# Kernel optimization log

Hardware: AMD Instinct MI355X
Metric: run time of the kernel (lower is better)

## Reference

```python
import jax, jax.numpy as jnp
import numpy as np

WAVE_LEN = 1000.0
DIM_G = 64


def box_relational_embedding(boxes):
    # boxes: (B, N, 4) -> (B, N, N, 64) trigonometric geometry embedding
    B, N, _ = boxes.shape
    x_min, y_min, x_max, y_max = jnp.split(boxes, 4, axis=-1)  # each (B,N,1)
    cx = (x_min + x_max) * 0.5
    cy = (y_min + y_max) * 0.5
    w = (x_max - x_min) + 1.0
    h = (y_max - y_min) + 1.0
    cxT = jnp.swapaxes(cx, 1, 2)  # (B,1,N)
    cyT = jnp.swapaxes(cy, 1, 2)
    dx = jnp.log(jnp.clip(jnp.abs((cx - cxT) / w), 1e-3))  # (B,N,N)
    dy = jnp.log(jnp.clip(jnp.abs((cy - cyT) / h), 1e-3))
    dw = jnp.log(w / jnp.swapaxes(w, 1, 2))
    dh = jnp.log(h / jnp.swapaxes(h, 1, 2))
    pos = jnp.stack([dx, dy, dw, dh], axis=-1)  # (B,N,N,4)
    n_freq = DIM_G // 8  # 8 frequency bands
    dim_mat = 1.0 / (WAVE_LEN ** (jnp.arange(n_freq, dtype=pos.dtype) / n_freq))
    mul = (100.0 * pos)[..., None] * dim_mat  # (B,N,N,4,8)
    mul = mul.reshape(B, N, N, 4 * n_freq)  # (B,N,N,32)
    return jnp.concatenate([jnp.sin(mul), jnp.cos(mul)], axis=-1)  # (B,N,N,64)


def setup_inputs() -> dict:
    key = jax.random.key(0)
    ks = jax.random.split(key, 12)
    B, N, D, H = 32, 196, 1024, 8
    scale = 0.02
    inp = {
        "input_query": jax.random.normal(ks[0], (B, N, D), jnp.float32),
        "input_key": jax.random.normal(ks[1], (B, N, D), jnp.float32),
        "input_value": jax.random.normal(ks[2], (B, N, D), jnp.float32),
        "input_box": jax.random.uniform(ks[3], (B, N, 4), jnp.float32),
        "Wq": jax.random.normal(ks[4], (D, D), jnp.float32) * scale,
        "bq": jnp.zeros((D,), jnp.float32),
        "Wk": jax.random.normal(ks[5], (D, D), jnp.float32) * scale,
        "bk": jnp.zeros((D,), jnp.float32),
        "Wv": jax.random.normal(ks[6], (D, D), jnp.float32) * scale,
        "bv": jnp.zeros((D,), jnp.float32),
        "Wo": jax.random.normal(ks[7], (D, D), jnp.float32) * scale,
        "bo": jnp.zeros((D,), jnp.float32),
        "WG_w": jax.random.normal(ks[8], (H, DIM_G), jnp.float32) * scale,  # 8 stacked (64->1) linears
        "WG_b": jnp.zeros((H,), jnp.float32),
    }
    return inp


def reference(input_query, input_key, input_value, input_box,
              Wq, bq, Wk, bk, Wv, bv, Wo, bo, WG_w, WG_b):
    B, N, D = input_query.shape
    H = WG_w.shape[0]
    dk = D // H
    # relation geometry weights per head: (B,H,N,N)
    geo = box_relational_embedding(input_box)  # (B,N,N,64)
    wg = jax.nn.relu(jnp.einsum('bnmg,hg->bhnm', geo, WG_w) + WG_b[None, :, None, None])
    # projections (torch Linear: x @ W.T + b), reshape to (B,H,N,dk)
    def proj(x, W, b):
        return (x @ W.T + b).reshape(B, N, H, dk).transpose(0, 2, 1, 3)
    q = proj(input_query, Wq, bq)
    k = proj(input_key, Wk, bk)
    v = proj(input_value, Wv, bv)
    scores = jnp.einsum('bhnd,bhmd->bhnm', q, k) / np.sqrt(dk).astype(q.dtype)
    logits = jnp.log(jnp.clip(wg, 1e-6)) + scores
    attn = jax.nn.softmax(logits, axis=-1)  # (B,H,N,N)
    out = jnp.einsum('bhnm,bhmd->bhnd', attn, v)  # (B,H,N,dk)
    out = out.transpose(0, 2, 1, 3).reshape(B, N, D)
    return out @ Wo.T + bo
```

## Files before the change

kernel.cpp:

```cpp
#include <hip/hip_runtime.h>
#include <hip/hip_bf16.h>

typedef __bf16 bf16;
typedef _Float16 half_t;
typedef bf16 bf16x8 __attribute__((ext_vector_type(8)));
typedef bf16 bf16x4 __attribute__((ext_vector_type(4)));
typedef float floatx4 __attribute__((ext_vector_type(4)));

#define B_ 32
#define N_ 196
#define H_ 8
#define D_ 1024
#define DK_ 128
#define BN_ (B_ * N_)
#define BH_ (B_ * H_)
#define NPAD_ 224
#define PSTRIDE_ 232

#define KT3_ 32

typedef __attribute__((address_space(3))) unsigned int lds_uint;
typedef const __attribute__((address_space(1))) unsigned int glb_uint;

__device__ __forceinline__ void async_copy16(const bf16* g, bf16* l) {
  __builtin_amdgcn_global_load_lds((glb_uint*)g, (lds_uint*)l, 16, 0, 0);
}

#define BARRIER() asm volatile("s_barrier" ::: "memory")
#define WAITV0() asm volatile("s_waitcnt vmcnt(0)" ::: "memory")
#define WAITV4() asm volatile("s_waitcnt vmcnt(4)" ::: "memory")

__global__ __launch_bounds__(256) void cvt3_kernel(const float* __restrict__ s0,
                                                   const float* __restrict__ s1,
                                                   const float* __restrict__ s2,
                                                   bf16* __restrict__ d0,
                                                   bf16* __restrict__ d1,
                                                   bf16* __restrict__ d2, int n4) {
  const int which = blockIdx.y;
  const float* s = (which == 0) ? s0 : (which == 1) ? s1 : s2;
  bf16* d = (which == 0) ? d0 : (which == 1) ? d1 : d2;
  int i = blockIdx.x * 256 + threadIdx.x;
  if (i >= n4) return;
  float4 v = ((const float4*)s)[i];
  bf16x4 o;
  o[0] = (bf16)v.x;
  o[1] = (bf16)v.y;
  o[2] = (bf16)v.z;
  o[3] = (bf16)v.w;
  *(bf16x4*)(d + (size_t)i * 4) = o;
}

__global__ __launch_bounds__(256) void cvt4_kernel(const float* __restrict__ s0,
                                                   const float* __restrict__ s1,
                                                   const float* __restrict__ s2,
                                                   const float* __restrict__ s3,
                                                   bf16* __restrict__ d0,
                                                   bf16* __restrict__ d1,
                                                   bf16* __restrict__ d2,
                                                   bf16* __restrict__ d3, int n4) {
  const int which = blockIdx.y;
  const float* s = (which == 0) ? s0 : (which == 1) ? s1 : (which == 2) ? s2 : s3;
  bf16* d = (which == 0) ? d0 : (which == 1) ? d1 : (which == 2) ? d2 : d3;
  int i = blockIdx.x * 256 + threadIdx.x;
  if (i >= n4) return;
  float4 v = ((const float4*)s)[i];
  bf16x4 o;
  o[0] = (bf16)v.x;
  o[1] = (bf16)v.y;
  o[2] = (bf16)v.z;
  o[3] = (bf16)v.w;
  *(bf16x4*)(d + (size_t)i * 4) = o;
}

__global__ __launch_bounds__(256) void geo_kernel(const float* __restrict__ box,
                                                  const float* __restrict__ WGw,
                                                  const float* __restrict__ WGb,
                                                  half_t* __restrict__ S) {
  __shared__ float4 wsh[128];
  if (threadIdx.x < 128) wsh[threadIdx.x] = ((const float4*)WGw)[threadIdx.x];
  __syncthreads();

  int tid = blockIdx.x * 256 + threadIdx.x;
  int b = tid / (N_ * N_);
  int rem = tid - b * (N_ * N_);
  int n = rem / N_;
  int m = rem - n * N_;

  float4 bn = ((const float4*)box)[b * N_ + n];
  float4 bm = ((const float4*)box)[b * N_ + m];
  float cxn = (bn.x + bn.z) * 0.5f, cyn = (bn.y + bn.w) * 0.5f;
  float wn = bn.z - bn.x + 1.0f, hn = bn.w - bn.y + 1.0f;
  float cxm = (bm.x + bm.z) * 0.5f, cym = (bm.y + bm.w) * 0.5f;
  float wm = bm.z - bm.x + 1.0f, hm = bm.w - bm.y + 1.0f;

  float pos[4];
  pos[0] = __logf(fmaxf(fabsf((cxn - cxm) / wn), 1e-3f));
  pos[1] = __logf(fmaxf(fabsf((cyn - cym) / hn), 1e-3f));
  pos[2] = __logf(wn / wm);
  pos[3] = __logf(hn / hm);

  const float dims[8] = {1.0f,          0.4216965034f, 0.1778279410f, 0.0749894209f,
                         0.0316227766f, 0.0133352143f, 0.0056234133f, 0.0023713737f};
  float feat[64];
#pragma unroll
  for (int p = 0; p < 4; p++) {
#pragma unroll
    for (int f = 0; f < 8; f++) {
      float a = 100.0f * pos[p] * dims[f];
      feat[p * 8 + f] = __sinf(a);
      feat[32 + p * 8 + f] = __cosf(a);
    }
  }
#pragma unroll
  for (int hh = 0; hh < 8; hh++) {
    float accv = WGb[hh];
#pragma unroll
    for (int g4 = 0; g4 < 16; g4++) {
      float4 wv = wsh[hh * 16 + g4];
      accv += feat[g4 * 4 + 0] * wv.x + feat[g4 * 4 + 1] * wv.y +
              feat[g4 * 4 + 2] * wv.z + feat[g4 * 4 + 3] * wv.w;
    }
    S[((size_t)((b * H_ + hh) * N_ + n)) * NPAD_ + m] = (half_t)fmaxf(accv, 1e-6f);
  }
}

template <int VARIANT>
__global__ __launch_bounds__(256, 3) void gemm3b(
    const bf16* __restrict__ A0, const bf16* __restrict__ A1, const bf16* __restrict__ A2,
    const bf16* __restrict__ W0, const bf16* __restrict__ W1, const bf16* __restrict__ W2,
    const float* __restrict__ b0, const float* __restrict__ b1, const float* __restrict__ b2,
    void* __restrict__ O0, void* __restrict__ O1, void* __restrict__ O2) {
  __shared__ bf16 As[3][128 * 32];
  __shared__ bf16 Bs[3][128 * 32];

  const int z = (VARIANT == 0) ? blockIdx.z : 0;
  const bf16* A = (z == 0) ? A0 : (z == 1) ? A1 : A2;
  const bf16* W = (z == 0) ? W0 : (z == 1) ? W1 : W2;
  const float* bias = (z == 0) ? b0 : (z == 1) ? b1 : b2;

  const int tid = threadIdx.x;
  const int lane = tid & 63;
  const int wid = tid >> 6;
  const int l16 = lane & 15;
  const int quad = lane >> 4;
  const int wm = wid >> 1;
  const int wn = wid & 1;

  const bf16* gA = A + (size_t)blockIdx.y * 128 * D_;
  const bf16* gB = W + (size_t)blockIdx.x * 128 * D_;

  size_t sOff[2];
  int sDst[2];
#pragma unroll
  for (int u = 0; u < 2; u++) {
    const int slot = u * 256 + tid;
    const int srow = slot >> 2;
    const int scs = slot & 3;
    sOff[u] = (size_t)srow * D_ + (size_t)((scs ^ (srow & 3)) * 8);
    sDst[u] = slot * 8;
  }

  int arow[4], brow[4];
#pragma unroll
  for (int i = 0; i < 4; i++) arow[i] = (wm * 64 + i * 16 + l16) * 32;
#pragma unroll
  for (int j = 0; j < 4; j++) brow[j] = (wn * 64 + j * 16 + l16) * 32;
  const int kslot = (quad ^ (l16 & 3)) * 8;

  floatx4 acc[4][4];
#pragma unroll
  for (int i = 0; i < 4; i++)
#pragma unroll
    for (int j = 0; j < 4; j++)
#pragma unroll
      for (int r = 0; r < 4; r++) acc[i][j][r] = 0.0f;

#pragma unroll
  for (int kt = 0; kt < 2; kt++) {
    const bf16* sa = gA + kt * 32;
    const bf16* sb = gB + kt * 32;
#pragma unroll
    for (int u = 0; u < 2; u++) {
      async_copy16(sa + sOff[u], &As[kt][sDst[u]]);
      async_copy16(sb + sOff[u], &Bs[kt][sDst[u]]);
    }
  }
  WAITV4();
  BARRIER();

  for (int kt = 0; kt < KT3_; ++kt) {
    const int g = kt % 3;
    const bool pf = (kt + 2 < KT3_);
    if (pf) {
      const int gn = (kt + 2) % 3;
      const bf16* pa = gA + (kt + 2) * 32;
      const bf16* pb = gB + (kt + 2) * 32;
#pragma unroll
      for (int u = 0; u < 2; u++) {
        async_copy16(pa + sOff[u], &As[gn][sDst[u]]);
        async_copy16(pb + sOff[u], &Bs[gn][sDst[u]]);
      }
    }
    const bf16* Ab = As[g];
    const bf16* Bb = Bs[g];
    bf16x8 af[4], bfv[4];
#pragma unroll
    for (int i = 0; i < 4; i++) af[i] = *(const bf16x8*)(Ab + arow[i] + kslot);
#pragma unroll
    for (int j = 0; j < 4; j++) bfv[j] = *(const bf16x8*)(Bb + brow[j] + kslot);
    __builtin_amdgcn_s_setprio(1);
#pragma unroll
    for (int i = 0; i < 4; i++)
#pragma unroll
      for (int j = 0; j < 4; j++)
        acc[i][j] = __builtin_amdgcn_mfma_f32_16x16x32_bf16(af[i], bfv[j], acc[i][j], 0, 0, 0);
    __builtin_amdgcn_s_setprio(0);
    if (kt < KT3_ - 1) {
      if (pf) WAITV4();
      else    WAITV0();
      BARRIER();
    }
  }

  const int m0 = blockIdx.y * 128 + wm * 64;
  const int n0 = blockIdx.x * 128 + wn * 64;
#pragma unroll
  for (int j = 0; j < 4; j++) {
    const int col = n0 + j * 16 + l16;
    const float bv = bias[col];
#pragma unroll
    for (int i = 0; i < 4; i++) {
#pragma unroll
      for (int r = 0; r < 4; r++) {
        const int row = m0 + i * 16 + quad * 4 + r;
        float v = acc[i][j][r] + bv;
        if (VARIANT == 1) {
          ((float*)O0)[(size_t)row * D_ + col] = v;
        } else if (z < 2) {
          bf16* Cout = z ? (bf16*)O1 : (bf16*)O0;
          Cout[(size_t)row * D_ + col] = (bf16)v;
        } else {
          int b = row / N_;
          int n = row - b * N_;
          int h = col >> 7;
          int d = col & (DK_ - 1);
          ((bf16*)O2)[((size_t)((b * H_ + h) * DK_ + d)) * NPAD_ + n] = (bf16)v;
        }
      }
    }
  }
}

__global__ __launch_bounds__(256) void attn_kernel(const bf16* __restrict__ Q,
                                                   const bf16* __restrict__ Kmat,
                                                   const bf16* __restrict__ Vt,
                                                   const half_t* __restrict__ Sb,
                                                   bf16* __restrict__ AO) {
  __shared__ alignas(16) char smem[46080];
  bf16* KsB[2] = {(bf16*)smem, (bf16*)smem + 4096};
  bf16* Pl = (bf16*)smem;
  bf16* VsB[2] = {(bf16*)(smem + 29696), (bf16*)(smem + 29696) + 4096};

  const int f = blockIdx.x;
  const int tile = (f >> 3) & 3;
  const int bh = (f & 7) | ((f >> 5) << 3);
  const int b = bh >> 3;
  const int h = bh & 7;
  const int tid = threadIdx.x;
  const int wave = tid >> 6;
  const int lane = tid & 63;
  const int l16 = lane & 15;
  const int quad = lane >> 4;
  const int nrb = tile * 64 + wave * 16;

  size_t kSrc[2];
  int kDst[2];
#pragma unroll
  for (int u = 0; u < 2; u++) {
    const int slot = u * 256 + tid;
    const int srow = slot >> 4;
    const int scs = slot & 15;
    kSrc[u] = (size_t)(b * N_ + srow) * D_ + h * DK_ + (scs ^ (srow & 7)) * 8;
    kDst[u] = slot * 8;
  }
  size_t vSrc[2];
#pragma unroll
  for (int u = 0; u < 2; u++) {
    const int slot = u * 256 + tid;
    const int vrow = slot >> 2;
    const int vcs = slot & 3;
    vSrc[u] = (size_t)bh * DK_ * NPAD_ + (size_t)vrow * NPAD_ + (vcs ^ (vrow & 3)) * 8;
  }

#pragma unroll
  for (int u = 0; u < 2; u++) async_copy16(Kmat + kSrc[u], KsB[0] + kDst[u]);

  const int na = nrb + l16;
  const bool nav = na < N_;
  const bf16* aptr = Q + ((size_t)(b * N_ + (nav ? na : 0))) * D_ + h * DK_ + quad * 8;
  bf16x8 afr[4];
#pragma unroll
  for (int kk = 0; kk < 4; kk++) {
    bf16x8 v = *(const bf16x8*)(aptr + kk * 32);
    if (!nav) {
#pragma unroll
      for (int e = 0; e < 8; e++) v[e] = (bf16)0.0f;
    }
    afr[kk] = v;
  }
  WAITV0();
  BARRIER();

  floatx4 S[14];
#pragma unroll
  for (int j = 0; j < 14; j++)
#pragma unroll
    for (int r = 0; r < 4; r++) S[j][r] = 0.0f;

  for (int jt = 0; jt < 7; ++jt) {
    const int cur = jt & 1;
    if (jt < 6) {
      const size_t koff = (size_t)((jt + 1) * 32) * D_;
#pragma unroll
      for (int u = 0; u < 2; u++)
        async_copy16(Kmat + kSrc[u] + koff, KsB[cur ^ 1] + kDst[u]);
    }
    const bf16* Kb = KsB[cur];
    __builtin_amdgcn_s_setprio(1);
#pragma unroll
    for (int jj = 0; jj < 2; jj++) {
      const int mloc = jj * 16 + l16;
#pragma unroll
      for (int kk = 0; kk < 4; kk++) {
        bf16x8 bb = *(const bf16x8*)(Kb + mloc * 128 + ((kk * 4 + quad) ^ (l16 & 7)) * 8);
        S[jt * 2 + jj] = __builtin_amdgcn_mfma_f32_16x16x32_bf16(afr[kk], bb, S[jt * 2 + jj], 0, 0, 0);
      }
    }
    __builtin_amdgcn_s_setprio(0);
    if (jt < 6) {
      WAITV0();
      BARRIER();
    }
  }

#pragma unroll
  for (int u = 0; u < 2; u++) async_copy16(Vt + vSrc[u], VsB[0] + kDst[u]);

  BARRIER();

  const float scale = 0.08838834764831845f;
  const half_t* bbase = Sb + ((size_t)bh * N_) * NPAD_;
  bf16* pw = Pl + wave * 16 * PSTRIDE_;
  float inv[4];
#pragma unroll
  for (int r = 0; r < 4; r++) {
    const int n = nrb + quad * 4 + r;
    const bool nv = n < N_;
    const size_t brow = (size_t)(nv ? n : 0) * NPAD_;
    float mx = -1e30f;
#pragma unroll
    for (int j = 0; j < 14; j++) {
      const int m = j * 16 + l16;
      float s = (nv && m < N_) ? S[j][r] * scale : -1e30f;
      S[j][r] = s;
      mx = fmaxf(mx, s);
    }
#pragma unroll
    for (int off = 1; off < 16; off <<= 1) mx = fmaxf(mx, __shfl_xor(mx, off, 64));
    float sum = 0.0f;
#pragma unroll
    for (int j = 0; j < 14; j++) {
      const int m = j * 16 + l16;
      float w = (m < N_) ? (float)bbase[brow + m] : 0.0f;
      float e = w * __expf(S[j][r] - mx);
      sum += e;
      pw[(quad * 4 + r) * PSTRIDE_ + m] = (bf16)e;
    }
#pragma unroll
    for (int off = 1; off < 16; off <<= 1) sum += __shfl_xor(sum, off, 64);
    inv[r] = 1.0f / sum;
  }
  __syncthreads();

  floatx4 O[8];
#pragma unroll
  for (int j2 = 0; j2 < 8; j2++)
#pragma unroll
    for (int r = 0; r < 4; r++) O[j2][r] = 0.0f;

  const bf16* pr = pw + l16 * PSTRIDE_ + quad * 8;
  for (int t7 = 0; t7 < 7; ++t7) {
    const int cur = t7 & 1;
    if (t7 < 6) {
      const size_t voff = (size_t)((t7 + 1) * 32);
#pragma unroll
      for (int u = 0; u < 2; u++)
        async_copy16(Vt + vSrc[u] + voff, VsB[cur ^ 1] + kDst[u]);
    }
    const bf16* Vb = VsB[cur];
    bf16x8 a = *(const bf16x8*)(pr + t7 * 32);
    __builtin_amdgcn_s_setprio(1);
#pragma unroll
    for (int j2 = 0; j2 < 8; j2++) {
      bf16x8 bb = *(const bf16x8*)(Vb + (j2 * 16 + l16) * 32 + (quad ^ (l16 & 3)) * 8);
      O[j2] = __builtin_amdgcn_mfma_f32_16x16x32_bf16(a, bb, O[j2], 0, 0, 0);
    }
    __builtin_amdgcn_s_setprio(0);
    if (t7 < 6) {
      WAITV0();
      BARRIER();
    }
  }

#pragma unroll
  for (int r = 0; r < 4; r++) {
    const int n = nrb + quad * 4 + r;
    if (n < N_) {
#pragma unroll
      for (int j2 = 0; j2 < 8; j2++) {
        AO[((size_t)(b * N_ + n)) * D_ + h * DK_ + j2 * 16 + l16] = (bf16)(O[j2][r] * inv[r]);
      }
    }
  }
}

extern "C" void kernel_launch(void* const* d_in, const int* in_sizes, int n_in,
                              void* d_out, int out_size, void* d_ws, size_t ws_size,
                              hipStream_t stream) {
  const float* xq = (const float*)d_in[0];
  const float* xk = (const float*)d_in[1];
  const float* xv = (const float*)d_in[2];
  const float* box = (const float*)d_in[3];
  const float* Wq = (const float*)d_in[4];
  const float* bq = (const float*)d_in[5];
  const float* Wk = (const float*)d_in[6];
  const float* bk = (const float*)d_in[7];
  const float* Wv = (const float*)d_in[8];
  const float* bv = (const float*)d_in[9];
  const float* Wo = (const float*)d_in[10];
  const float* bo = (const float*)d_in[11];
  const float* WGw = (const float*)d_in[12];
  const float* WGb = (const float*)d_in[13];

  size_t off = 0;
  char* wsc = (char*)d_ws;
  auto alloc = [&](size_t bytes) -> void* {
    void* p = wsc + off;
    off += (bytes + 255) & ~(size_t)255;
    return p;
  };
  bf16* xq_b = (bf16*)alloc((size_t)BN_ * D_ * 2);
  bf16* xk_b = (bf16*)alloc((size_t)BN_ * D_ * 2);
  bf16* xv_b = (bf16*)alloc((size_t)BN_ * D_ * 2);
  bf16* wq_b = (bf16*)alloc((size_t)D_ * D_ * 2);
  bf16* wk_b = (bf16*)alloc((size_t)D_ * D_ * 2);
  bf16* wv_b = (bf16*)alloc((size_t)D_ * D_ * 2);
  bf16* wo_b = (bf16*)alloc((size_t)D_ * D_ * 2);
  bf16* q_b = (bf16*)alloc((size_t)BN_ * D_ * 2);
  bf16* k_b = (bf16*)alloc((size_t)BN_ * D_ * 2);
  bf16* vt_b = (bf16*)alloc((size_t)BH_ * DK_ * NPAD_ * 2);
  bf16* ao_b = (bf16*)alloc((size_t)BN_ * D_ * 2);
  half_t* S = (half_t*)alloc((size_t)BH_ * N_ * NPAD_ * 2);

  const int n4x = BN_ * D_ / 4;
  const int n4w = D_ * D_ / 4;
  dim3 g3(n4x / 256, 3, 1);
  cvt3_kernel<<<g3, 256, 0, stream>>>(xq, xk, xv, xq_b, xk_b, xv_b, n4x);
  dim3 g4(n4w / 256, 4, 1);
  cvt4_kernel<<<g4, 256, 0, stream>>>(Wq, Wk, Wv, Wo, wq_b, wk_b, wv_b, wo_b, n4w);

  geo_kernel<<<(B_ * N_ * N_) / 256, 256, 0, stream>>>(box, WGw, WGb, S);

  hipMemsetAsync(vt_b, 0, (size_t)BH_ * DK_ * NPAD_ * 2, stream);

  dim3 gqkv(D_ / 128, BN_ / 128, 3);
  gemm3b<0><<<gqkv, 256, 0, stream>>>(xq_b, xk_b, xv_b, wq_b, wk_b, wv_b, bq, bk, bv,
                                      q_b, k_b, vt_b);

  attn_kernel<<<1024, 256, 0, stream>>>(q_b, k_b, vt_b, S, ao_b);

  dim3 gout(D_ / 128, BN_ / 128, 1);
  gemm3b<1><<<gout, 256, 0, stream>>>(ao_b, nullptr, nullptr, wo_b, nullptr, nullptr,
                                      bo, nullptr, nullptr, d_out, nullptr, nullptr);
}
```

Measured before the change: 320.0 us.

## Rework GEMM pipeline to double-buffered K=64 tiles with XCD-aware block remap

The projection GEMMs drop the triple-buffered K=32 pipeline in favour of double-buffered K=64 tiles. That halves the number of barrier and wait rounds, and the next tile's global-to-LDS copies are split across the two MFMA halves of each iteration. Blocks are also remapped so that consecutive hardware block IDs, which are dealt round-robin across XCDs, land on contiguous tile ranges, aiming at better L2 reuse. The cost is more LDS per block and lower occupancy (launch bounds drop from 3 to 2 blocks per CU), plus a full vmcnt(0) wait each iteration.

Measured after the change: 315.0 us. Within noise of the previous version (-1.6%).

```diff
diff --git a/kernel.cpp b/kernel.cpp
--- a/kernel.cpp
+++ b/kernel.cpp
@@ -17,7 +17,7 @@
 #define NPAD_ 224
 #define PSTRIDE_ 232
 
-#define KT3_ 32
+#define KT_ 16
 
 typedef __attribute__((address_space(3))) unsigned int lds_uint;
 typedef const __attribute__((address_space(1))) unsigned int glb_uint;
@@ -28,7 +28,6 @@
 
 #define BARRIER() asm volatile("s_barrier" ::: "memory")
 #define WAITV0() asm volatile("s_waitcnt vmcnt(0)" ::: "memory")
-#define WAITV4() asm volatile("s_waitcnt vmcnt(4)" ::: "memory")
 
 __global__ __launch_bounds__(256) void cvt3_kernel(const float* __restrict__ s0,
                                                    const float* __restrict__ s1,
@@ -125,15 +124,23 @@
 }
 
 template <int VARIANT>
-__global__ __launch_bounds__(256, 3) void gemm3b(
+__global__ __launch_bounds__(256, 2) void gemm2p(
     const bf16* __restrict__ A0, const bf16* __restrict__ A1, const bf16* __restrict__ A2,
     const bf16* __restrict__ W0, const bf16* __restrict__ W1, const bf16* __restrict__ W2,
     const float* __restrict__ b0, const float* __restrict__ b1, const float* __restrict__ b2,
     void* __restrict__ O0, void* __restrict__ O1, void* __restrict__ O2) {
-  __shared__ bf16 As[3][128 * 32];
-  __shared__ bf16 Bs[3][128 * 32];
-
-  const int z = (VARIANT == 0) ? blockIdx.z : 0;
+  __shared__ bf16 As[2][128 * 64];
+  __shared__ bf16 Bs[2][128 * 64];
+
+  const int NZ = (VARIANT == 0) ? 3 : 1;
+  const int chunk = 49 * NZ;
+  const int f = blockIdx.x + (blockIdx.y << 3) + blockIdx.z * 392;
+  const int L = (f & 7) * chunk + (f >> 3);
+  const int lx = L & 7;
+  const int lyz = L >> 3;
+  const int ly = (VARIANT == 0) ? (lyz % 49) : lyz;
+  const int z = (VARIANT == 0) ? (lyz / 49) : 0;
+
   const bf16* A = (z == 0) ? A0 : (z == 1) ? A1 : A2;
   const bf16* W = (z == 0) ? W0 : (z == 1) ? W1 : W2;
   const float* bias = (z == 0) ? b0 : (z == 1) ? b1 : b2;
@@ -146,26 +153,22 @@
   const int wm = wid >> 1;
   const int wn = wid & 1;
 
-  const bf16* gA = A + (size_t)blockIdx.y * 128 * D_;
-  const bf16* gB = W + (size_t)blockIdx.x * 128 * D_;
-
-  size_t sOff[2];
-  int sDst[2];
-#pragma unroll
-  for (int u = 0; u < 2; u++) {
-    const int slot = u * 256 + tid;
-    const int srow = slot >> 2;
-    const int scs = slot & 3;
-    sOff[u] = (size_t)srow * D_ + (size_t)((scs ^ (srow & 3)) * 8);
-    sDst[u] = slot * 8;
-  }
-
-  int arow[4], brow[4];
-#pragma unroll
-  for (int i = 0; i < 4; i++) arow[i] = (wm * 64 + i * 16 + l16) * 32;
-#pragma unroll
-  for (int j = 0; j < 4; j++) brow[j] = (wn * 64 + j * 16 + l16) * 32;
-  const int kslot = (quad ^ (l16 & 3)) * 8;
+  const bf16* gA = A + (size_t)ly * 128 * D_;
+  const bf16* gB = W + (size_t)lx * 128 * D_;
+
+  const int srow = tid >> 3;
+  const int lslot = (tid & 7) ^ (srow & 7);
+  size_t sOff[4];
+#pragma unroll
+  for (int u = 0; u < 4; u++) sOff[u] = (size_t)(u * 32 + srow) * D_ + lslot * 8;
+
+  int arow[4], brow[4], kslot[2];
+#pragma unroll
+  for (int i = 0; i < 4; i++) arow[i] = (wm * 64 + i * 16 + l16) * 64;
+#pragma unroll
+  for (int j = 0; j < 4; j++) brow[j] = (wn * 64 + j * 16 + l16) * 64;
+#pragma unroll
+  for (int kk = 0; kk < 2; kk++) kslot[kk] = ((kk * 4 + quad) ^ (l16 & 7)) * 8;
 
   floatx4 acc[4][4];
 #pragma unroll
@@ -176,38 +179,32 @@
       for (int r = 0; r < 4; r++) acc[i][j][r] = 0.0f;
 
 #pragma unroll
-  for (int kt = 0; kt < 2; kt++) {
-    const bf16* sa = gA + kt * 32;
-    const bf16* sb = gB + kt * 32;
-#pragma unroll
-    for (int u = 0; u < 2; u++) {
-      async_copy16(sa + sOff[u], &As[kt][sDst[u]]);
-      async_copy16(sb + sOff[u], &Bs[kt][sDst[u]]);
-    }
-  }
-  WAITV4();
+  for (int u = 0; u < 4; u++) {
+    async_copy16(gA + sOff[u], &As[0][u * 2048 + tid * 8]);
+    async_copy16(gB + sOff[u], &Bs[0][u * 2048 + tid * 8]);
+  }
+  WAITV0();
   BARRIER();
 
-  for (int kt = 0; kt < KT3_; ++kt) {
-    const int g = kt % 3;
-    const bool pf = (kt + 2 < KT3_);
+  for (int kt = 0; kt < KT_; ++kt) {
+    const int cur = kt & 1;
+    const bf16* Ab = As[cur];
+    const bf16* Bb = Bs[cur];
+    const bool pf = (kt + 1 < KT_);
+    const bf16* pa = gA + (kt + 1) * 64;
+    const bf16* pb = gB + (kt + 1) * 64;
+    bf16* dA = As[cur ^ 1];
+    bf16* dB = Bs[cur ^ 1];
+    bf16x8 af[4], bfv[4];
+
+#pragma unroll
+    for (int i = 0; i < 4; i++) af[i] = *(const bf16x8*)(Ab + arow[i] + kslot[0]);
+#pragma unroll
+    for (int j = 0; j < 4; j++) bfv[j] = *(const bf16x8*)(Bb + brow[j] + kslot[0]);
     if (pf) {
-      const int gn = (kt + 2) % 3;
-      const bf16* pa = gA + (kt + 2) * 32;
-      const bf16* pb = gB + (kt + 2) * 32;
-#pragma unroll
-      for (int u = 0; u < 2; u++) {
-        async_copy16(pa + sOff[u], &As[gn][sDst[u]]);
-        async_copy16(pb + sOff[u], &Bs[gn][sDst[u]]);
-      }
-    }
-    const bf16* Ab = As[g];
-    const bf16* Bb = Bs[g];
-    bf16x8 af[4], bfv[4];
-#pragma unroll
-    for (int i = 0; i < 4; i++) af[i] = *(const bf16x8*)(Ab + arow[i] + kslot);
-#pragma unroll
-    for (int j = 0; j < 4; j++) bfv[j] = *(const bf16x8*)(Bb + brow[j] + kslot);
+#pragma unroll
+      for (int u = 0; u < 4; u++) async_copy16(pa + sOff[u], dA + u * 2048 + tid * 8);
+    }
     __builtin_amdgcn_s_setprio(1);
 #pragma unroll
     for (int i = 0; i < 4; i++)
@@ -215,15 +212,31 @@
       for (int j = 0; j < 4; j++)
         acc[i][j] = __builtin_amdgcn_mfma_f32_16x16x32_bf16(af[i], bfv[j], acc[i][j], 0, 0, 0);
     __builtin_amdgcn_s_setprio(0);
-    if (kt < KT3_ - 1) {
-      if (pf) WAITV4();
-      else    WAITV0();
+
+#pragma unroll
+    for (int i = 0; i < 4; i++) af[i] = *(const bf16x8*)(Ab + arow[i] + kslot[1]);
+#pragma unroll
+    for (int j = 0; j < 4; j++) bfv[j] = *(const bf16x8*)(Bb + brow[j] + kslot[1]);
+    if (pf) {
+#pragma unroll
+      for (int u = 0; u < 4; u++) async_copy16(pb + sOff[u], dB + u * 2048 + tid * 8);
+    }
+    __builtin_amdgcn_s_setprio(1);
+#pragma unroll
+    for (int i = 0; i < 4; i++)
+#pragma unroll
+      for (int j = 0; j < 4; j++)
+        acc[i][j] = __builtin_amdgcn_mfma_f32_16x16x32_bf16(af[i], bfv[j], acc[i][j], 0, 0, 0);
+    __builtin_amdgcn_s_setprio(0);
+
+    if (pf) {
+      WAITV0();
       BARRIER();
     }
   }
 
-  const int m0 = blockIdx.y * 128 + wm * 64;
-  const int n0 = blockIdx.x * 128 + wn * 64;
+  const int m0 = ly * 128 + wm * 64;
+  const int n0 = lx * 128 + wn * 64;
 #pragma unroll
   for (int j = 0; j < 4; j++) {
     const int col = n0 + j * 16 + l16;
@@ -474,12 +487,12 @@
   hipMemsetAsync(vt_b, 0, (size_t)BH_ * DK_ * NPAD_ * 2, stream);
 
   dim3 gqkv(D_ / 128, BN_ / 128, 3);
-  gemm3b<0><<<gqkv, 256, 0, stream>>>(xq_b, xk_b, xv_b, wq_b, wk_b, wv_b, bq, bk, bv,
+  gemm2p<0><<<gqkv, 256, 0, stream>>>(xq_b, xk_b, xv_b, wq_b, wk_b, wv_b, bq, bk, bv,
                                       q_b, k_b, vt_b);
 
   attn_kernel<<<1024, 256, 0, stream>>>(q_b, k_b, vt_b, S, ao_b);
 
   dim3 gout(D_ / 128, BN_ / 128, 1);
-  gemm3b<1><<<gout, 256, 0, stream>>>(ao_b, nullptr, nullptr, wo_b, nullptr, nullptr,
+  gemm2p<1><<<gout, 256, 0, stream>>>(ao_b, nullptr, nullptr, wo_b, nullptr, nullptr,
                                       bo, nullptr, nullptr, d_out, nullptr, nullptr);
 }
```
